# Kernel tuning notes

Hardware: AMD Instinct MI355X
Metric: run time of the kernel (lower is better)

The kernel has to match this reference:

```python
import jax, jax.numpy as jnp
import numpy as np

INPUT_DIM = 1024
LATENT_DIM = 16 * INPUT_DIM
K_VALUES = (32, 128, 256)


def setup_inputs() -> dict:
    key = jax.random.key(0)
    ks = jax.random.split(key, 7)
    B = 4096
    x = jax.random.normal(ks[0], (B, INPUT_DIM), dtype=jnp.float32)
    MLP_output = jax.random.normal(ks[1], (B, INPUT_DIM), dtype=jnp.float32)
    # encoder: nn.Linear(input_dim, latent_dim) -> weight [latent, input], bias zeroed in __init__
    W_enc = jax.random.normal(ks[2], (LATENT_DIM, INPUT_DIM), dtype=jnp.float32) / np.sqrt(INPUT_DIM)
    b_enc = jnp.zeros((LATENT_DIM,), dtype=jnp.float32)
    # decoder / skip / b_dec are zeros in __init__, but use small random values so the
    # reference exercises non-trivial math (zeros would make decode degenerate)
    W_dec = jax.random.normal(ks[3], (LATENT_DIM, INPUT_DIM), dtype=jnp.float32) * 0.02
    b_dec = jax.random.normal(ks[4], (INPUT_DIM,), dtype=jnp.float32) * 0.02
    W_skip = jax.random.normal(ks[5], (INPUT_DIM, INPUT_DIM), dtype=jnp.float32) * 0.02
    return {"x": x, "MLP_output": MLP_output, "W_enc": W_enc, "b_enc": b_enc,
            "W_dec": W_dec, "b_dec": b_dec, "W_skip": W_skip}


def _topk_relu(z, k):
    # keep top-k per row, relu the kept values, zero elsewhere (scatter)
    vals, idx = jax.lax.top_k(z, k)                     # [B, k]
    vals = jax.nn.relu(vals)
    rows = jnp.arange(z.shape[0])[:, None]              # [B, 1]
    return jnp.zeros_like(z).at[rows, idx].set(vals)


def reference(x, MLP_output, W_enc, b_enc, W_dec, b_dec, W_skip):
    B = x.shape[0]
    pre = x @ W_enc.T + b_enc                            # [B, latent] (shared across k)
    skip = x @ W_skip + b_dec                            # [B, input]
    total_variance = jnp.sum((x - x.mean(0)) ** 2)

    mean_encoded = jnp.zeros((B, LATENT_DIM), dtype=x.dtype)
    mean_decoded = jnp.zeros((B, INPUT_DIM), dtype=x.dtype)
    total_loss = jnp.asarray(0.0, dtype=x.dtype)
    encoded = None
    for k in K_VALUES:                                   # fixed small set of k values
        encoded = _topk_relu(pre, k)                     # [B, latent]
        decoded = encoded @ W_dec + skip                 # [B, input]
        mean_encoded = mean_encoded + encoded
        mean_decoded = mean_decoded + decoded
        total_loss = total_loss + jnp.sum((MLP_output - decoded) ** 2)

    n = float(len(K_VALUES))
    mean_encoded = mean_encoded / n
    mean_decoded = mean_decoded / n
    total_loss = total_loss / total_variance
    # l0 over the last (k=256) encoded tensor
    l0_norm_final = jnp.sum(jnp.count_nonzero(encoded, axis=0))
    return (mean_encoded, mean_decoded, total_loss, l0_norm_final)
```

## Files before the change

kernel.cpp:

```cpp
#include <hip/hip_runtime.h>
#include <stdint.h>

typedef short   bf16x8 __attribute__((ext_vector_type(8)));
typedef float   f32x4  __attribute__((ext_vector_type(4)));
typedef unsigned short u16x8 __attribute__((ext_vector_type(8)));
typedef unsigned long long u64;
typedef long long i64;
typedef long long i64x2 __attribute__((ext_vector_type(2)));

#define B_ROWS 4096
#define D_IN   1024
#define L_DIM  16384
#define NBIN   2048
#define CCAP   1024
#define SLOTS  32
#define W8SCALE 1200.0f

__device__ __forceinline__ unsigned short f2bf(float f) {
  unsigned int u = __float_as_uint(f);
  u = (u + 0x7FFFu + ((u >> 16) & 1u)) >> 16;
  return (unsigned short)u;
}
__device__ __forceinline__ float bf2f(unsigned short h) {
  return __uint_as_float(((unsigned int)h) << 16);
}
__device__ __forceinline__ unsigned char f2e4m3(float v) {
  unsigned int u = __float_as_uint(v);
  unsigned int s = (u >> 24) & 0x80u;
  unsigned int a = u & 0x7FFFFFFFu;
  unsigned int r = (a + 0x0007FFFFu + ((a >> 20) & 1u)) >> 20;
  if (r <= (120u << 3)) return (unsigned char)s;
  r -= (120u << 3);
  if (r > 0x7Eu) r = 0x7Eu;
  return (unsigned char)(s | r);
}
__device__ __forceinline__ float e4m3f(unsigned char b) {
  unsigned int e = (b >> 3) & 0xFu, m = b & 7u, s = ((unsigned int)b & 0x80u) << 24;
  if (e == 0) return __uint_as_float(s);
  return __uint_as_float(s | ((e + 120u) << 23) | (m << 20));
}
__device__ __forceinline__ unsigned int sortkey(float f) {
  unsigned int u = __float_as_uint(f);
  return (u & 0x80000000u) ? ~u : (u | 0x80000000u);
}
__device__ __forceinline__ float keyval(unsigned int k) {
  unsigned int u = (k & 0x80000000u) ? (k & 0x7FFFFFFFu) : ~k;
  return __uint_as_float(u);
}
__device__ __forceinline__ int binof(float v) {
  int b = (int)((v + 2.0f) * (2048.0f / 7.0f));
  return b < 0 ? 0 : (b > 2047 ? 2047 : b);
}
__device__ __forceinline__ void gl_lds16(const void* g, void* l) {
  __builtin_amdgcn_global_load_lds(
      (const __attribute__((address_space(1))) unsigned int*)g,
      (__attribute__((address_space(3))) unsigned int*)l, 16, 0, 0);
}
__device__ __forceinline__ float waveSum(float v) {
  #pragma unroll
  for (int m = 32; m; m >>= 1) v += __shfl_xor(v, m);
  return v;
}

__global__ void k_zero(float* scal, float* colsum, float* colsq, unsigned int* rowcnt) {
  int t = blockIdx.x * blockDim.x + threadIdx.x;
  if (t < 8) scal[t] = 0.f;
  if (t < 1024) { colsum[t] = 0.f; colsq[t] = 0.f; }
  for (int i = t; i < B_ROWS; i += gridDim.x * blockDim.x) rowcnt[i] = 0u;
}

__global__ void k_convert(const float* __restrict__ in, unsigned short* __restrict__ out, int n4) {
  int i = blockIdx.x * blockDim.x + threadIdx.x;
  int stride = gridDim.x * blockDim.x;
  for (; i < n4; i += stride) {
    f32x4 v = *((const f32x4*)in + i);
    ushort4 o;
    o.x = f2bf(v[0]); o.y = f2bf(v[1]); o.z = f2bf(v[2]); o.w = f2bf(v[3]);
    *((ushort4*)out + i) = o;
  }
}

__global__ void k_convert_fp8p(const float* __restrict__ in, unsigned char* __restrict__ out, int n4) {
  int i = blockIdx.x * blockDim.x + threadIdx.x;
  int stride = gridDim.x * blockDim.x;
  for (; i < n4; i += stride) {
    f32x4 v = *((const f32x4*)in + i);
    unsigned int u = 0;
    #pragma unroll
    for (int j = 0; j < 4; j++) u |= ((unsigned int)f2e4m3(v[j])) << (8 * j);
    int p = i * 4;
    int np = (p & ~63) + (((p >> 3) & 3) * 16) + (((p >> 5) & 1) * 8) + (p & 7);
    *(unsigned int*)&out[np] = u;
  }
}

__global__ void k_convert_i8(const float* __restrict__ in, unsigned int* __restrict__ out, int n4) {
  int i = blockIdx.x * blockDim.x + threadIdx.x;
  int stride = gridDim.x * blockDim.x;
  for (; i < n4; i += stride) {
    f32x4 v = *((const f32x4*)in + i);
    unsigned int u = 0;
    #pragma unroll
    for (int j = 0; j < 4; j++) {
      int q = (int)rintf(v[j] * W8SCALE);
      q = q > 127 ? 127 : (q < -127 ? -127 : q);
      u |= ((unsigned int)q & 0xFFu) << (8 * j);
    }
    out[i] = u;
  }
}

__global__ void k_transpose_bf(const float* __restrict__ in, unsigned short* __restrict__ out, int n) {
  __shared__ float tile[32][33];
  int bx = blockIdx.x * 32, by = blockIdx.y * 32;
  int tx = threadIdx.x, ty = threadIdx.y;
  tile[ty][tx] = in[(size_t)(by + ty) * n + bx + tx];
  __syncthreads();
  out[(size_t)(bx + ty) * n + by + tx] = f2bf(tile[tx][ty]);
}

__global__ __launch_bounds__(256) void k_var1(const float* __restrict__ x, float* colsum, float* colsq) {
  int g = blockIdx.x;
  int t = threadIdx.x;
  float s[4] = {0,0,0,0}, q[4] = {0,0,0,0};
  for (int r = 0; r < 32; r++) {
    const float* rp = x + (size_t)(g * 32 + r) * D_IN;
    #pragma unroll
    for (int j = 0; j < 4; j++) {
      float v = rp[t + 256 * j];
      s[j] += v; q[j] += v * v;
    }
  }
  #pragma unroll
  for (int j = 0; j < 4; j++) {
    atomicAdd(&colsum[t + 256 * j], s[j]);
    atomicAdd(&colsq [t + 256 * j], q[j]);
  }
}

__global__ __launch_bounds__(256) void k_var2(const float* colsum, const float* colsq, float* scal) {
  __shared__ float red[4];
  int t = threadIdx.x;
  float loc = 0.f;
  #pragma unroll
  for (int j = 0; j < 4; j++) {
    int c = t + 256 * j;
    float cs = colsum[c], cq = colsq[c];
    loc += cq - cs * cs * (1.f / (float)B_ROWS);
  }
  loc = waveSum(loc);
  if ((t & 63) == 0) red[t >> 6] = loc;
  __syncthreads();
  if (t == 0) scal[1] = red[0] + red[1] + red[2] + red[3];
}

__device__ __forceinline__ void stage_half8(const unsigned char* __restrict__ G,
                                            int Kb, int r0, int k0b,
                                            unsigned char* buf, int t) {
  #pragma unroll
  for (int j = 0; j < 2; j++) {
    int q = j * 256 + t;
    int row = q >> 2, u = q & 3;
    int uu = u ^ ((row >> 1) & 3);
    gl_lds16(&G[(size_t)(r0 + row) * Kb + k0b + uu * 16], &buf[q * 16]);
  }
}

__global__ __launch_bounds__(256, 3) void k_gemm_enc(
    const unsigned char* __restrict__ A8, const unsigned char* __restrict__ B8,
    const float* __restrict__ bias,
    u64* __restrict__ cand, unsigned int* __restrict__ rowcnt,
    int M, int N, int K) {
  __shared__ unsigned char sBuf[3 * 16384];
  unsigned int*  stageKey = (unsigned int*)sBuf;
  unsigned char* stageCol = (unsigned char*)&sBuf[16384];
  unsigned int*  s_cnt    = (unsigned int*)&sBuf[20480];
  unsigned int*  s_base   = (unsigned int*)&sBuf[21504];

  const int t = threadIdx.x;
  const int w = t >> 6, l = t & 63;
  const int wr = w >> 1, wc = w & 1;
  const int lm = l & 15, ku = l >> 4, lg = l >> 4;
  const int row0 = blockIdx.y * 128, col0 = blockIdx.x * 128;
  const int Kb = K;
  const int NT = K >> 6;

  f32x4 acc[4][4] = {};

  stage_half8(A8, Kb, row0, 0,   sBuf + 0,             t);
  stage_half8(B8, Kb, col0, 0,   sBuf + 8192,          t);
  stage_half8(A8, Kb, row0, 64,  sBuf + 16384,         t);
  stage_half8(B8, Kb, col0, 64,  sBuf + 16384 + 8192,  t);

  for (int tt = 0; tt < NT; tt++) {
    asm volatile("s_waitcnt vmcnt(4)" ::: "memory");
    __builtin_amdgcn_s_barrier();

    int ks = (tt + 2 < NT) ? (tt + 2) : (NT - 1);
    unsigned char* nb = sBuf + ((tt + 2) % 3) * 16384;
    stage_half8(A8, Kb, row0, ks * 64, nb, t);
    stage_half8(B8, Kb, col0, ks * 64, nb + 8192, t);

    const unsigned char* cb = sBuf + (tt % 3) * 16384;

    i64x2 bfr[4], af[4];
    #pragma unroll
    for (int n = 0; n < 4; n++) {
      int r = wc * 64 + n * 16 + lm;
      bfr[n] = *(const i64x2*)&cb[8192 + r * 64 + ((ku ^ ((r >> 1) & 3)) * 16)];
    }
    #pragma unroll
    for (int mm = 0; mm < 4; mm++) {
      int r = wr * 64 + mm * 16 + lm;
      af[mm] = *(const i64x2*)&cb[r * 64 + ((ku ^ ((r >> 1) & 3)) * 16)];
    }

    __builtin_amdgcn_s_setprio(1);
    #pragma unroll
    for (int c = 0; c < 2; c++)
      #pragma unroll
      for (int mm = 0; mm < 4; mm++)
        #pragma unroll
        for (int n = 0; n < 4; n++)
          acc[mm][n] = __builtin_amdgcn_mfma_f32_16x16x32_fp8_fp8(af[mm][c], bfr[n][c], acc[mm][n], 0, 0, 0);
    __builtin_amdgcn_s_setprio(0);
  }

  asm volatile("s_waitcnt vmcnt(0) lgkmcnt(0)" ::: "memory");
  __syncthreads();

  if (t < 128) s_cnt[t] = 0u;
  __syncthreads();

  #pragma unroll
  for (int n = 0; n < 4; n++) {
    int cl = wc * 64 + n * 16 + lm;
    float bv = bias[col0 + cl];
    #pragma unroll
    for (int m = 0; m < 4; m++) {
      int rloc = wr * 64 + m * 16 + lg * 4;
      #pragma unroll
      for (int j = 0; j < 4; j++) {
        float v = acc[m][n][j] + bv;
        if (v > 1.7f) {
          int r = rloc + j;
          unsigned int p = atomicAdd(&s_cnt[r], 1u);
          if (p < SLOTS) {
            stageKey[r * SLOTS + p] = sortkey(v);
            stageCol[r * SLOTS + p] = (unsigned char)cl;
          }
        }
      }
    }
  }
  __syncthreads();

  if (t < 128) {
    unsigned int c = s_cnt[t];
    if (c > SLOTS)      { atomicAdd(&rowcnt[row0 + t], 4096u); s_base[t] = 0x80000000u; }
    else if (c)         s_base[t] = atomicAdd(&rowcnt[row0 + t], c);
    else                s_base[t] = 0u;
  }
  __syncthreads();

  for (int s = t; s < 128 * SLOTS; s += 256) {
    int r = s >> 5, p = s & (SLOTS - 1);
    unsigned int c = s_cnt[r], g0 = s_base[r];
    if ((unsigned int)p < c && c <= SLOTS && !(g0 & 0x80000000u)) {
      unsigned int g = g0 + (unsigned int)p;
      if (g < CCAP)
        cand[(size_t)(row0 + r) * CCAP + g] =
            ((u64)stageKey[s] << 32) | (unsigned int)(~(unsigned int)(col0 + stageCol[s]));
    }
  }
}

__device__ __forceinline__ void stage_swz(const unsigned short* __restrict__ G, int ld,
                                          int r0, int k0, unsigned short* lds, int t) {
  #pragma unroll
  for (int j = 0; j < 4; j++) {
    int q = j * 256 + t;
    int row = q >> 3, u = q & 7;
    int uu = u ^ (row & 7);
    gl_lds16(&G[(size_t)(r0 + row) * ld + k0 + uu * 8], &lds[q * 8]);
  }
}

__device__ __forceinline__ void gemm_core(
    const unsigned short* __restrict__ A, const unsigned short* __restrict__ Bm,
    unsigned short* sA, unsigned short* sB,
    int row0, int col0, int K, int t, int wr, int wc, int lm, int u0,
    f32x4 acc[4][4]) {
  for (int k0 = 0; k0 < K; k0 += 64) {
    stage_swz(A,  K, row0, k0, sA, t);
    stage_swz(Bm, K, col0, k0, sB, t);
    __syncthreads();
    bf16x8 af[4][2], bfr[4][2];
    #pragma unroll
    for (int i = 0; i < 4; i++) {
      int r = wr * 64 + i * 16 + lm;
      int sw = r & 7;
      af[i][0] = *(const bf16x8*)&sA[r * 64 + ((u0 ^ sw) * 8)];
      af[i][1] = *(const bf16x8*)&sA[r * 64 + (((u0 + 4) ^ sw) * 8)];
    }
    #pragma unroll
    for (int n = 0; n < 4; n++) {
      int r = wc * 64 + n * 16 + lm;
      int sw = r & 7;
      bfr[n][0] = *(const bf16x8*)&sB[r * 64 + ((u0 ^ sw) * 8)];
      bfr[n][1] = *(const bf16x8*)&sB[r * 64 + (((u0 + 4) ^ sw) * 8)];
    }
    #pragma unroll
    for (int i = 0; i < 4; i++)
      #pragma unroll
      for (int n = 0; n < 4; n++) {
        acc[i][n] = __builtin_amdgcn_mfma_f32_16x16x32_bf16(af[i][0], bfr[n][0], acc[i][n], 0, 0, 0);
        acc[i][n] = __builtin_amdgcn_mfma_f32_16x16x32_bf16(af[i][1], bfr[n][1], acc[i][n], 0, 0, 0);
      }
    __syncthreads();
  }
}

__global__ __launch_bounds__(256) void k_gemm_skip(
    const unsigned short* __restrict__ A, const unsigned short* __restrict__ Bm,
    const float* __restrict__ bias, unsigned short* __restrict__ Cb,
    int M, int N, int K) {
  __shared__ unsigned short sA[128 * 64];
  __shared__ unsigned short sB[128 * 64];
  const int t = threadIdx.x;
  const int w = t >> 6, l = t & 63;
  const int wr = w >> 1, wc = w & 1;
  const int lm = l & 15, u0 = l >> 4;
  const int row0 = blockIdx.y * 128, col0 = blockIdx.x * 128;

  f32x4 acc[4][4] = {};
  gemm_core(A, Bm, sA, sB, row0, col0, K, t, wr, wc, lm, u0, acc);

  const int lg = l >> 4;
  #pragma unroll
  for (int n = 0; n < 4; n++) {
    int col = col0 + wc * 64 + n * 16 + lm;
    float bv = bias[col];
    #pragma unroll
    for (int i = 0; i < 4; i++) {
      int rbase = row0 + wr * 64 + i * 16 + lg * 4;
      #pragma unroll
      for (int j = 0; j < 4; j++)
        Cb[(size_t)(rbase + j) * N + col] = f2bf(acc[i][n][j] + bv);
    }
  }
}

__global__ __launch_bounds__(256) void k_select(
    const u64* __restrict__ cand, const unsigned int* __restrict__ rowcnt,
    const unsigned char* __restrict__ xf8, const unsigned char* __restrict__ wenc8,
    const float* __restrict__ benc,
    float* __restrict__ menc, uint2* __restrict__ lists, unsigned int* __restrict__ l0p) {
  __shared__ u64 sc[CCAP];
  __shared__ unsigned int hist[NBIN];
  __shared__ u64 scratch[256];
  __shared__ unsigned int sS[256];
  __shared__ uint2 win[256];
  __shared__ int s_bb[3];
  __shared__ unsigned int s_bc[3];
  __shared__ u64 s_T[3];
  __shared__ int s_scnt;
  __shared__ unsigned int s_l0, s_pos;

  const int b = blockIdx.x, t = threadIdx.x;
  float* rowp = menc + (size_t)b * L_DIM;

  int cnt = (int)rowcnt[b];
  if (cnt >= 256 && cnt <= CCAP) {
    for (int i = t; i < cnt; i += 256) sc[i] = cand[(size_t)b * CCAP + i];
    #pragma unroll 4
    for (int g = 0; g < 16; g++) {
      f32x4 z = {};
      *(f32x4*)&rowp[g * 1024 + t * 4] = z;
    }
    __syncthreads();
  } else {
    unsigned char* xrow = (unsigned char*)scratch;
    for (int i = t; i < D_IN; i += 256) xrow[i] = xf8[(size_t)b * D_IN + i];
    __syncthreads();
    for (int q = 0; q < 64; q++) {
      int lat = q * 256 + t;
      const unsigned char* wp = &wenc8[(size_t)lat * D_IN];
      float a = 0.f;
      for (int k = 0; k < D_IN; k++) a += e4m3f(xrow[k]) * e4m3f(wp[k]);
      rowp[lat] = a + benc[lat];
    }
    __syncthreads();
    float T = 1.7f;
    for (int at = 0; at < 10; at++) {
      if (t == 0) s_scnt = 0;
      __syncthreads();
      int loc = 0;
      for (int q = 0; q < 64; q++) loc += (rowp[q * 256 + t] > T) ? 1 : 0;
      atomicAdd(&s_scnt, loc);
      __syncthreads();
      int c2 = s_scnt;
      if (c2 >= 256 && c2 <= CCAP) break;
      T = (c2 < 256) ? (T - 0.5f) : (T + 0.3f);
      __syncthreads();
    }
    if (t == 0) s_scnt = 0;
    __syncthreads();
    for (int q = 0; q < 64; q++) {
      int lat = q * 256 + t;
      float v = rowp[lat];
      if (v > T) {
        int p = atomicAdd(&s_scnt, 1);
        if (p < CCAP) sc[p] = ((u64)sortkey(v) << 32) | (unsigned int)(~(unsigned int)lat);
      }
    }
    __syncthreads();
    cnt = min(s_scnt, CCAP);
    for (int i = t * 4; i < L_DIM; i += 1024) { f32x4 z = {}; *(f32x4*)&rowp[i] = z; }
    __syncthreads();
  }

  for (int i = t; i < NBIN; i += 256) hist[i] = 0u;
  __syncthreads();
  for (int i = t; i < cnt; i += 256) {
    float v = keyval((unsigned int)(sc[i] >> 32));
    atomicAdd(&hist[binof(v)], 1u);
  }
  __syncthreads();

  unsigned int csum = 0;
  #pragma unroll
  for (int j = 0; j < 8; j++) csum += hist[t * 8 + j];
  sS[t] = csum;
  __syncthreads();
  for (int off = 1; off < 256; off <<= 1) {
    unsigned int v2 = (t + off < 256) ? sS[t + off] : 0u;
    __syncthreads();
    sS[t] += v2;
    __syncthreads();
  }
  {
    unsigned int above = (t < 255) ? sS[t + 1] : 0u;
    unsigned int run = 0;
    for (int j = 7; j >= 0; j--) {
      int bb = t * 8 + j;
      unsigned int S = above + run, h = hist[bb];
      if (h) {
        if (S < 32u  && 32u  <= S + h) { s_bb[0] = bb; s_bc[0] = S; }
        if (S < 128u && 128u <= S + h) { s_bb[1] = bb; s_bc[1] = S; }
        if (S < 256u && 256u <= S + h) { s_bb[2] = bb; s_bc[2] = S; }
      }
      run += h;
    }
  }
  __syncthreads();

  for (int ri = 0; ri < 3; ri++) {
    const int r = (ri == 0) ? 32 : (ri == 1) ? 128 : 256;
    int bb = s_bb[ri];
    int cA = (int)s_bc[ri];
    if (t == 0) s_scnt = 0;
    __syncthreads();
    for (int i = t; i < cnt; i += 256) {
      float v = keyval((unsigned int)(sc[i] >> 32));
      if (binof(v) == bb) {
        int p = atomicAdd(&s_scnt, 1);
        if (p < 256) scratch[p] = sc[i];
      }
    }
    __syncthreads();
    int m = min(s_scnt, 256);
    for (int i = t; i < m; i += 256) {
      u64 me = scratch[i];
      int rk = 0;
      for (int j2 = 0; j2 < m; j2++) rk += (scratch[j2] > me) ? 1 : 0;
      if (rk == r - cA - 1) s_T[ri] = me;
    }
    __syncthreads();
  }

  if (t == 0) { s_pos = 0u; s_l0 = 0u; }
  __syncthreads();
  const u64 T32 = s_T[0], T128 = s_T[1], T256 = s_T[2];
  for (int i = t; i < cnt; i += 256) {
    u64 e = sc[i];
    int w = (e >= T32) ? 3 : (e >= T128) ? 2 : (e >= T256) ? 1 : 0;
    if (w) {
      unsigned int p = atomicAdd(&s_pos, 1u);
      int idx = (int)(~(unsigned int)e) & (L_DIM - 1);
      float v = keyval((unsigned int)(e >> 32));
      float rv = fmaxf(v, 0.f);
      if (p < 256u)
        win[p] = make_uint2((unsigned int)idx | ((unsigned int)w << 20), __float_as_uint(rv));
      if (rv > 0.f) atomicAdd(&s_l0, 1u);
    }
  }
  __syncthreads();
  for (int i = (int)s_pos + t; i < 256; i += 256) win[i] = make_uint2(0xFFFFFu, 0u);
  __syncthreads();

  for (int k = 2; k <= 256; k <<= 1) {
    for (int j = k >> 1; j > 0; j >>= 1) {
      int x = t ^ j;
      if (x > t) {
        uint2 a = win[t], bb2 = win[x];
        bool asc = ((t & k) == 0);
        bool swap = asc ? ((a.x & 0xFFFFFu) > (bb2.x & 0xFFFFFu))
                        : ((a.x & 0xFFFFFu) < (bb2.x & 0xFFFFFu));
        if (swap) { win[t] = bb2; win[x] = a; }
      }
      __syncthreads();
    }
  }

  lists[(size_t)b * 256 + t] = win[t];

  {
    uint2 e = win[t];
    int idx = (int)(e.x & 0xFFFFFu) & (L_DIM - 1);
    unsigned int wg = (e.x >> 20) & 3u;
    float rv = __uint_as_float(e.y);
    rowp[idx] = rv * (float)wg * (1.f / 3.f);
  }

  if (t == 0) atomicAdd(l0p, s_l0);
}

__global__ __launch_bounds__(512) void k_decode(
    const uint2* __restrict__ lists, const unsigned char* __restrict__ W8,
    const unsigned short* __restrict__ skipb, const float* __restrict__ mlp,
    float* __restrict__ mdec, float* __restrict__ loss_acc) {
  __shared__ uint2 ll[256];
  __shared__ float part[3][128][25];
  __shared__ float red[2];
  const int b = blockIdx.x, t = threadIdx.x;
  if (t < 256) ll[t] = lists[(size_t)b * 256 + t];
  __syncthreads();

  const int lane = t & 127, grp = t >> 7;
  const int c = lane * 8;

  float a1[8] = {}, a2[8] = {}, a3[8] = {};

  #pragma unroll 4
  for (int i = 0; i < 64; i++) {
    uint2 e = ll[4 * i + grp];
    int idx = (int)(e.x & 0xFFFFFu) & (L_DIM - 1);
    int wgt = (int)((e.x >> 20) & 3u);
    float v = __uint_as_float(e.y) * (1.0f / W8SCALE);
    uint2 qw = *(const uint2*)&W8[(size_t)idx * D_IN + c];
    float f[8];
    #pragma unroll
    for (int j = 0; j < 4; j++) {
      f[j]     = (float)((int)(qw.x << (24 - 8 * j)) >> 24);
      f[4 + j] = (float)((int)(qw.y << (24 - 8 * j)) >> 24);
    }
    if (wgt == 3) {
      #pragma unroll
      for (int j = 0; j < 8; j++) a1[j] += v * f[j];
    } else if (wgt == 2) {
      #pragma unroll
      for (int j = 0; j < 8; j++) a2[j] += v * f[j];
    } else {
      #pragma unroll
      for (int j = 0; j < 8; j++) a3[j] += v * f[j];
    }
  }

  if (grp != 0) {
    #pragma unroll
    for (int j = 0; j < 8; j++) {
      part[grp - 1][lane][j]      = a1[j];
      part[grp - 1][lane][8 + j]  = a2[j];
      part[grp - 1][lane][16 + j] = a3[j];
    }
  }
  __syncthreads();

  float lsum = 0.f;
  if (grp == 0) {
    #pragma unroll
    for (int g = 0; g < 3; g++) {
      #pragma unroll
      for (int j = 0; j < 8; j++) {
        a1[j] += part[g][lane][j];
        a2[j] += part[g][lane][8 + j];
        a3[j] += part[g][lane][16 + j];
      }
    }
    u16x8 skv = *(const u16x8*)&skipb[(size_t)b * D_IN + c];
    f32x4 m0 = *(const f32x4*)&mlp[(size_t)b * D_IN + c];
    f32x4 m1 = *(const f32x4*)&mlp[(size_t)b * D_IN + c + 4];
    float mm[8] = {m0[0], m0[1], m0[2], m0[3], m1[0], m1[1], m1[2], m1[3]};
    float md[8];
    #pragma unroll
    for (int j = 0; j < 8; j++) {
      float sk   = bf2f(skv[j]);
      float d32  = sk + a1[j];
      float d128 = d32 + a2[j];
      float d256 = d128 + a3[j];
      md[j] = (d32 + d128 + d256) * (1.f / 3.f);
      float e1 = mm[j] - d32, e2 = mm[j] - d128, e3 = mm[j] - d256;
      lsum += e1 * e1 + e2 * e2 + e3 * e3;
    }
    f32x4 o0 = {md[0], md[1], md[2], md[3]};
    f32x4 o1 = {md[4], md[5], md[6], md[7]};
    *(f32x4*)&mdec[(size_t)b * D_IN + c]     = o0;
    *(f32x4*)&mdec[(size_t)b * D_IN + c + 4] = o1;
  }

  lsum = waveSum(lsum);
  if ((t & 63) == 0 && t < 128) red[t >> 6] = lsum;
  __syncthreads();
  if (t == 0) atomicAdd(loss_acc, red[0] + red[1]);
}

__global__ void k_final(const float* scal, const unsigned int* l0p, float* outscal) {
  outscal[0] = scal[0] / scal[1];
  outscal[1] = (float)(*l0p);
}

extern "C" void kernel_launch(void* const* d_in, const int* in_sizes, int n_in,
                              void* d_out, int out_size, void* d_ws, size_t ws_size,
                              hipStream_t stream) {
  (void)in_sizes; (void)n_in; (void)out_size; (void)ws_size;
  const float* x     = (const float*)d_in[0];
  const float* mlp   = (const float*)d_in[1];
  const float* Wenc  = (const float*)d_in[2];
  const float* benc  = (const float*)d_in[3];
  const float* Wdec  = (const float*)d_in[4];
  const float* bdec  = (const float*)d_in[5];
  const float* Wskip = (const float*)d_in[6];

  char* ws = (char*)d_ws;
  float*          scal    = (float*)(ws + 0);
  unsigned int*   l0p     = (unsigned int*)(ws + 8);
  float*          colsum  = (float*)(ws + 256);
  float*          colsq   = (float*)(ws + 4352);
  unsigned int*   rowcnt  = (unsigned int*)(ws + 8448);
  unsigned short* xb      = (unsigned short*)(ws + 24832);
  unsigned char*  wenc8   = (unsigned char*)(ws + 8413440);
  unsigned char*  xf8     = (unsigned char*)(ws + 8413440 + 16777216);
  unsigned short* wsktb   = (unsigned short*)(ws + 41967872);
  unsigned short* skipb   = (unsigned short*)(ws + 44065024);
  uint2*          lists   = (uint2*)(ws + 52453632);
  u64*            cand    = (u64*)(ws + 60842240);
  unsigned char*  wdec8   = (unsigned char*)(ws + 60842240);

  float* out  = (float*)d_out;
  float* menc = out;
  float* mdec = out + (size_t)B_ROWS * L_DIM;
  float* oscl = out + (size_t)B_ROWS * L_DIM + (size_t)B_ROWS * D_IN;

  k_zero<<<16, 256, 0, stream>>>(scal, colsum, colsq, rowcnt);
  k_convert<<<2048, 256, 0, stream>>>(x, xb, (B_ROWS * D_IN) / 4);
  k_convert_fp8p<<<1024, 256, 0, stream>>>(x,    xf8,   (B_ROWS * D_IN) / 4);
  k_convert_fp8p<<<2048, 256, 0, stream>>>(Wenc, wenc8, (L_DIM * D_IN) / 4);
  k_transpose_bf<<<dim3(32, 32), dim3(32, 32), 0, stream>>>(Wskip, wsktb, D_IN);
  k_var1<<<128, 256, 0, stream>>>(x, colsum, colsq);
  k_var2<<<1, 256, 0, stream>>>(colsum, colsq, scal);
  k_gemm_enc<<<dim3(L_DIM / 128, B_ROWS / 128), 256, 0, stream>>>(
      xf8, wenc8, benc, cand, rowcnt, B_ROWS, L_DIM, D_IN);
  k_gemm_skip<<<dim3(D_IN / 128, B_ROWS / 128), 256, 0, stream>>>(
      xb, wsktb, bdec, skipb, B_ROWS, D_IN, D_IN);
  k_select<<<B_ROWS, 256, 0, stream>>>(cand, rowcnt, xf8, wenc8, benc, menc, lists, l0p);
  k_convert_i8<<<2048, 256, 0, stream>>>(Wdec, (unsigned int*)wdec8, (L_DIM * D_IN) / 4);
  k_decode<<<B_ROWS, 512, 0, stream>>>(lists, wdec8, skipb, mlp, mdec, scal);
  k_final<<<1, 1, 0, stream>>>(scal, l0p, oscl);
}
```

Before: 486.4 us.

## Use scaled 32x32x64 fp8 MFMA for encoder GEMM with plain fp8 layout

Replaces the encoder GEMM's 16x16x32 fp8 MFMA tiling with the gfx950 mfma_scale 32x32x64 f8f6f4 instruction, using unit scales, and reorganises accumulators and the LDS fragment loads to match. The fp8 conversion kernel drops its k-permutation and writes a plain row-major layout. The epilogue is remapped to the 32x32 accumulator layout. The aim is higher matrix-core throughput and fewer instructions in the dominant GEMM. The risk is a mismatch if other kernels that read the fp8 buffers depended on the old permuted layout.

```diff
diff --git a/kernel.cpp b/kernel.cpp
--- a/kernel.cpp
+++ b/kernel.cpp
@@ -3,6 +3,9 @@
 
 typedef short   bf16x8 __attribute__((ext_vector_type(8)));
 typedef float   f32x4  __attribute__((ext_vector_type(4)));
+typedef float   f32x16 __attribute__((ext_vector_type(16)));
+typedef int     i32x4  __attribute__((ext_vector_type(4)));
+typedef int     i32x8  __attribute__((ext_vector_type(8)));
 typedef unsigned short u16x8 __attribute__((ext_vector_type(8)));
 typedef unsigned long long u64;
 typedef long long i64;
@@ -80,7 +83,7 @@
   }
 }
 
-__global__ void k_convert_fp8p(const float* __restrict__ in, unsigned char* __restrict__ out, int n4) {
+__global__ void k_convert_fp8(const float* __restrict__ in, unsigned char* __restrict__ out, int n4) {
   int i = blockIdx.x * blockDim.x + threadIdx.x;
   int stride = gridDim.x * blockDim.x;
   for (; i < n4; i += stride) {
@@ -88,9 +91,7 @@
     unsigned int u = 0;
     #pragma unroll
     for (int j = 0; j < 4; j++) u |= ((unsigned int)f2e4m3(v[j])) << (8 * j);
-    int p = i * 4;
-    int np = (p & ~63) + (((p >> 3) & 3) * 16) + (((p >> 5) & 1) * 8) + (p & 7);
-    *(unsigned int*)&out[np] = u;
+    *((unsigned int*)out + i) = u;
   }
 }
 
@@ -180,18 +181,25 @@
   const int t = threadIdx.x;
   const int w = t >> 6, l = t & 63;
   const int wr = w >> 1, wc = w & 1;
-  const int lm = l & 15, ku = l >> 4, lg = l >> 4;
+  const int lr = l & 31, lh = l >> 5;
   const int row0 = blockIdx.y * 128, col0 = blockIdx.x * 128;
   const int Kb = K;
   const int NT = K >> 6;
 
-  f32x4 acc[4][4] = {};
+  f32x16 acc[2][2] = {};
 
   stage_half8(A8, Kb, row0, 0,   sBuf + 0,             t);
   stage_half8(B8, Kb, col0, 0,   sBuf + 8192,          t);
   stage_half8(A8, Kb, row0, 64,  sBuf + 16384,         t);
   stage_half8(B8, Kb, col0, 64,  sBuf + 16384 + 8192,  t);
 
+  const int raf = wr * 64 + lr,  swa = (raf >> 1) & 3;
+  const int rbf = wc * 64 + lr,  swb = (rbf >> 1) & 3;
+  const int uA0 = ((2 * lh)     ^ swa) * 16, uA1 = ((2 * lh + 1) ^ swa) * 16;
+  const int uB0 = ((2 * lh)     ^ swb) * 16, uB1 = ((2 * lh + 1) ^ swb) * 16;
+  const int offA0 = raf * 64,        offA1 = (raf + 32) * 64;
+  const int offB0 = 8192 + rbf * 64, offB1 = 8192 + (rbf + 32) * 64;
+
   for (int tt = 0; tt < NT; tt++) {
     asm volatile("s_waitcnt vmcnt(4)" ::: "memory");
     __builtin_amdgcn_s_barrier();
@@ -203,26 +211,27 @@
 
     const unsigned char* cb = sBuf + (tt % 3) * 16384;
 
-    i64x2 bfr[4], af[4];
-    #pragma unroll
-    for (int n = 0; n < 4; n++) {
-      int r = wc * 64 + n * 16 + lm;
-      bfr[n] = *(const i64x2*)&cb[8192 + r * 64 + ((ku ^ ((r >> 1) & 3)) * 16)];
-    }
-    #pragma unroll
-    for (int mm = 0; mm < 4; mm++) {
-      int r = wr * 64 + mm * 16 + lm;
-      af[mm] = *(const i64x2*)&cb[r * 64 + ((ku ^ ((r >> 1) & 3)) * 16)];
-    }
+    union Frag { i32x8 w; i32x4 h[2]; };
+    Frag av[2], bv[2];
+    av[0].h[0] = *(const i32x4*)&cb[offA0 + uA0];
+    av[0].h[1] = *(const i32x4*)&cb[offA0 + uA1];
+    av[1].h[0] = *(const i32x4*)&cb[offA1 + uA0];
+    av[1].h[1] = *(const i32x4*)&cb[offA1 + uA1];
+    bv[0].h[0] = *(const i32x4*)&cb[offB0 + uB0];
+    bv[0].h[1] = *(const i32x4*)&cb[offB0 + uB1];
+    bv[1].h[0] = *(const i32x4*)&cb[offB1 + uB0];
+    bv[1].h[1] = *(const i32x4*)&cb[offB1 + uB1];
 
     __builtin_amdgcn_s_setprio(1);
     #pragma unroll
-    for (int c = 0; c < 2; c++)
-      #pragma unroll
-      for (int mm = 0; mm < 4; mm++)
-        #pragma unroll
-        for (int n = 0; n < 4; n++)
-          acc[mm][n] = __builtin_amdgcn_mfma_f32_16x16x32_fp8_fp8(af[mm][c], bfr[n][c], acc[mm][n], 0, 0, 0);
+    for (int mt = 0; mt < 2; mt++)
+      #pragma unroll
+      for (int nt = 0; nt < 2; nt++)
+        acc[mt][nt] = __builtin_amdgcn_mfma_scale_f32_32x32x64_f8f6f4(
+            av[mt].w, bv[nt].w, acc[mt][nt],
+            0, 0,
+            0, 0x7F7F7F7Fu,
+            0, 0x7F7F7F7Fu);
     __builtin_amdgcn_s_setprio(0);
   }
 
@@ -233,17 +242,17 @@
   __syncthreads();
 
   #pragma unroll
-  for (int n = 0; n < 4; n++) {
-    int cl = wc * 64 + n * 16 + lm;
-    float bv = bias[col0 + cl];
-    #pragma unroll
-    for (int m = 0; m < 4; m++) {
-      int rloc = wr * 64 + m * 16 + lg * 4;
-      #pragma unroll
-      for (int j = 0; j < 4; j++) {
-        float v = acc[m][n][j] + bv;
+  for (int nt = 0; nt < 2; nt++) {
+    int cl = wc * 64 + nt * 32 + lr;
+    float bvs = bias[col0 + cl];
+    #pragma unroll
+    for (int mt = 0; mt < 2; mt++) {
+      int rbase = wr * 64 + mt * 32 + lh * 4;
+      #pragma unroll
+      for (int i = 0; i < 16; i++) {
+        float v = acc[mt][nt][i] + bvs;
         if (v > 1.7f) {
-          int r = rloc + j;
+          int r = rbase + (i & 3) + 8 * (i >> 2);
           unsigned int p = atomicAdd(&s_cnt[r], 1u);
           if (p < SLOTS) {
             stageKey[r * SLOTS + p] = sortkey(v);
@@ -654,8 +663,8 @@
 
   k_zero<<<16, 256, 0, stream>>>(scal, colsum, colsq, rowcnt);
   k_convert<<<2048, 256, 0, stream>>>(x, xb, (B_ROWS * D_IN) / 4);
-  k_convert_fp8p<<<1024, 256, 0, stream>>>(x,    xf8,   (B_ROWS * D_IN) / 4);
-  k_convert_fp8p<<<2048, 256, 0, stream>>>(Wenc, wenc8, (L_DIM * D_IN) / 4);
+  k_convert_fp8<<<1024, 256, 0, stream>>>(x,    xf8,   (B_ROWS * D_IN) / 4);
+  k_convert_fp8<<<2048, 256, 0, stream>>>(Wenc, wenc8, (L_DIM * D_IN) / 4);
   k_transpose_bf<<<dim3(32, 32), dim3(32, 32), 0, stream>>>(Wskip, wsktb, D_IN);
   k_var1<<<128, 256, 0, stream>>>(x, colsum, colsq);
   k_var2<<<1, 256, 0, stream>>>(colsum, colsq, scal);
```

After: 488.8 us. No clear change (+0.5%).
